# Kernel tuning notes

Hardware: AMD Instinct MI355X
Metric: run time of the kernel (lower is better)

## Reference

```python
import jax, jax.numpy as jnp
import numpy as np
from jax import lax

NH, K, V, TOPK = 8, 64, 64, 4  # n_heads, key_size, val_size, SparseAttention top_k(=3+1)
EPS = 1e-7
BN_EPS = 1e-5


def conv1x1(x, w, b):
    # x: [B,C,H,W], w: [O,C] -> [B,O,H,W]
    return jnp.einsum('oc,bchw->bohw', w, x) + b[None, :, None, None]


def conv3x3(x, w, b):
    y = lax.conv_general_dilated(x, w, (1, 1), 'SAME',
                                 dimension_numbers=('NCHW', 'OIHW', 'NCHW'))
    return y + b[None, :, None, None]


def batchnorm(x, g, b):
    # training-mode BN over (N,H,W), biased variance (matches torch BatchNorm2d in train)
    m = jnp.mean(x, axis=(0, 2, 3), keepdims=True)
    v = jnp.var(x, axis=(0, 2, 3), keepdims=True)
    return (x - m) * lax.rsqrt(v + BN_EPS) * g[None, :, None, None] + b[None, :, None, None]


def to_flat(y, d):
    # [B, NH*d, H, W] -> [B*H*W*NH, d]
    B, _, H, W = y.shape
    return y.reshape(B, NH, d, H, W).transpose(0, 3, 4, 1, 2).reshape(B * H * W * NH, d)


def setup_inputs() -> dict:
    key = jax.random.key(0)
    ks = jax.random.split(key, 16)
    L, C, B, H, W = 4, 256, 8, 32, 32
    KH, VH = K * NH, V * NH
    s = 0.02
    return {
        'x': jax.random.normal(ks[0], (B, C, H, W), jnp.float32),
        'kw': jax.random.normal(ks[1], (L, KH, C), jnp.float32) * s,
        'kb': jax.random.normal(ks[2], (L, KH), jnp.float32) * s,
        'qw': jax.random.normal(ks[3], (L, KH, C), jnp.float32) * s,
        'qb': jax.random.normal(ks[4], (L, KH), jnp.float32) * s,
        'vw': jax.random.normal(ks[5], (L, VH, C), jnp.float32) * s,
        'vb': jax.random.normal(ks[6], (L, VH), jnp.float32) * s,
        'ow1': jax.random.normal(ks[7], (L, C, VH, 3, 3), jnp.float32) * s,
        'ob1': jax.random.normal(ks[8], (L, C), jnp.float32) * s,
        'bn_g': jnp.ones((L, C), jnp.float32),
        'bn_b': jnp.zeros((L, C), jnp.float32),
        'ow2': jax.random.normal(ks[9], (L, C, C, 3, 3), jnp.float32) * s,
        'ob2': jax.random.normal(ks[10], (L, C), jnp.float32) * s,
        'gammas': jax.random.normal(ks[11], (L,), jnp.float32),
    }


def reference(x, kw, kb, qw, qb, vw, vb, ow1, ob1, bn_g, bn_b, ow2, ob2, gammas):
    B, C, H, W = x.shape
    L = kw.shape[0]
    temp = jnp.asarray(np.power(K, 0.5), x.dtype)  # concentration=0.5
    keys, vals = [], []
    for l in range(L):  # structurally distinct layers: growing key/val list
        keys.append(to_flat(conv1x1(x, kw[l], kb[l]), K))  # [N,K]
        vals.append(to_flat(conv1x1(x, vw[l], vb[l]), V))  # [N,V]
        q = to_flat(conv1x1(x, qw[l], qb[l]), K)           # [N,K]
        kt = jnp.stack(keys + [jnp.zeros_like(keys[0])], axis=1)  # [N,T,K] zero key appended
        vt = jnp.stack(vals + [jnp.zeros_like(vals[0])], axis=1)  # [N,T,V]
        scores = jnp.einsum('nk,ntk->nt', q / temp, kt)
        attn = jax.nn.softmax(scores, axis=-1)
        T = attn.shape[1]
        if T > TOPK:  # SparseAttention: topk threshold, clamp, renormalize
            delta = lax.top_k(attn, TOPK)[0][:, -1] + EPS
            wgt = jnp.maximum(attn - delta[:, None], 0.0)
            attn = wgt / (jnp.sum(wgt, axis=1, keepdims=True) + EPS)
        o = jnp.einsum('nt,ntv->nv', attn, vt)  # [N,V]
        o = o.reshape(B, H, W, NH * V).transpose(0, 3, 1, 2)  # [B, NH*V, H, W]
        h1 = jax.nn.relu(batchnorm(conv3x3(o, ow1[l], ob1[l]), bn_g[l], bn_b[l]))
        h2 = conv3x3(h1, ow2[l], ob2[l])
        x = x + h2 * gammas[l]
    return x
```

## Files before the change

### kernel.cpp

```cpp
#include <hip/hip_runtime.h>


typedef __attribute__((ext_vector_type(8))) short short8;
typedef __attribute__((ext_vector_type(4))) float f32x4;
typedef __attribute__((ext_vector_type(4))) unsigned short ushort4_t;
typedef __attribute__((ext_vector_type(4))) unsigned int uint4_t;

#define NTOK 65536
#define NPIX 8192

__device__ __forceinline__ float bf2f(unsigned short u) {
  unsigned int v = ((unsigned int)u) << 16;
  float f; __builtin_memcpy(&f, &v, 4); return f;
}
__device__ __forceinline__ unsigned short f2bf(float f) {
  unsigned int u; __builtin_memcpy(&u, &f, 4);
  u = (u + 0x7FFFu + ((u >> 16) & 1u)) >> 16;
  return (unsigned short)u;
}
__device__ __forceinline__ float blo(unsigned int u) {
  unsigned int v = u << 16; float f; __builtin_memcpy(&f, &v, 4); return f;
}
__device__ __forceinline__ float bhi(unsigned int u) {
  unsigned int v = u & 0xFFFF0000u; float f; __builtin_memcpy(&f, &v, 4); return f;
}

__device__ __forceinline__ void gl_lds16(const unsigned short* g, const unsigned short* l) {
  __builtin_amdgcn_global_load_lds(
      (const __attribute__((address_space(1))) unsigned int*)g,
      (__attribute__((address_space(3))) unsigned int*)l, 16, 0, 0);
}

__global__ void k_prep(const float* __restrict__ kw, const float* __restrict__ vw,
                       const float* __restrict__ qw, const float* __restrict__ ow1,
                       const float* __restrict__ ow2, const float* __restrict__ kb,
                       const float* __restrict__ vb, const float* __restrict__ qb,
                       unsigned short* __restrict__ wkqv, unsigned short* __restrict__ w1,
                       unsigned short* __restrict__ w2, float* __restrict__ biascat) {
  long i = (long)blockIdx.x * 256 + threadIdx.x;
  if (i < 1572864) {
    int idx = (int)(i & 131071); int sl = (int)(i >> 17); int slot = sl % 3, l = sl / 3;
    const float* s = slot == 0 ? kw : slot == 1 ? vw : qw;
    wkqv[i] = f2bf(s[(size_t)l * 131072 + idx]);
    return;
  }
  i -= 1572864;
  if (i < 4718592) {
    int c = (int)(i % 512), tap = (int)((i / 512) % 9); long m = i / 4608;
    w1[i] = f2bf(ow1[(m * 512 + c) * 9 + tap]);
    return;
  }
  i -= 4718592;
  if (i < 2359296) {
    int c = (int)(i % 256), tap = (int)((i / 256) % 9); long m = i / 2304;
    w2[i] = f2bf(ow2[(m * 256 + c) * 9 + tap]);
    return;
  }
  i -= 2359296;
  if (i < 6144) {
    int o = (int)(i & 511); int sl = (int)(i >> 9); int slot = sl % 3, l = sl / 3;
    const float* s = slot == 0 ? kb : slot == 1 ? vb : qb;
    biascat[i] = s[l * 512 + o];
  }
}

__global__ __launch_bounds__(256) void k_x2cl(const float* __restrict__ src,
                                              unsigned short* __restrict__ dst) {
  __shared__ unsigned short t[64][68];
  const int hw0 = blockIdx.x * 64, b = blockIdx.y;
  const int tid = threadIdx.x;
  for (int cc = 0; cc < 4; cc++) {
    __syncthreads();
    {
      const int px = tid & 63, c = tid >> 6;
      #pragma unroll
      for (int i = 0; i < 16; i++)
        t[px][c + i * 4] = f2bf(src[((size_t)b * 256 + cc * 64 + c + i * 4) * 1024 + hw0 + px]);
    }
    __syncthreads();
    {
      const int px = tid >> 2, c0 = (tid & 3) * 16;
      unsigned short* dp = dst + ((size_t)b * 1024 + hw0 + px) * 256 + cc * 64 + c0;
      short8 v0, v1;
      #pragma unroll
      for (int i = 0; i < 8; i++) { v0[i] = (short)t[px][c0 + i]; v1[i] = (short)t[px][c0 + 8 + i]; }
      *(short8*)dp = v0; *(short8*)(dp + 8) = v1;
    }
  }
}

template<int MODE, int NSTEP, int KDIM, int CIN>
__global__ __launch_bounds__(256) void k_gemm(
    const unsigned short* __restrict__ W,
    const unsigned short* __restrict__ act,
    const float* __restrict__ bias,
    int l,
    unsigned short* __restrict__ ktok, unsigned short* __restrict__ vtok,
    unsigned short* __restrict__ qtok,
    float* __restrict__ pout) {
  __shared__ unsigned short sm[2][2][8192];

  const int bid = blockIdx.x;
  int m0, b, pix0, s;
  if constexpr (MODE == 0) {
    const int xcd = bid & 7, li = bid >> 3;
    const int nt = xcd * 8 + (li & 7);
    m0 = (li >> 3) * 128; s = 0;
    b = nt >> 3; pix0 = (nt & 7) * 128;
  } else {
    const int xcd = bid & 7, li = bid >> 3;
    const int nt = xcd * 8 + (li & 7);
    const int r = li >> 3;
    m0 = (r & 1) * 128; s = r >> 1;
    b = nt >> 3; pix0 = (nt & 7) * 128;
  }
  constexpr int SW = (MODE == 1) ? 128 : 64;

  const int tid = threadIdx.x;
  const int wid = tid >> 6, lane = tid & 63;
  const int lr = lane & 15, lg = lane >> 4;
  const int m_off = (wid >> 1) * 64, n_off = (wid & 1) * 64;

  const unsigned short* gA[4];
  const unsigned short* gB[4];
  #pragma unroll
  for (int j = 0; j < 4; j++) {
    const int o = (wid * 4 + j) * 512 + lane * 8;
    const int row = o >> 6;
    const int ksw = (((o >> 3) & 7) ^ (row & 7)) * 8;
    gA[j] = W + (size_t)(m0 + row) * KDIM + (MODE ? s * SW : 0) + ksw;
    if constexpr (MODE == 0) {
      gB[j] = act + ((size_t)b * 1024 + pix0 + row) * 256 + ksw;
    } else {
      const int pix = pix0 + row, py = pix >> 5, px = pix & 31;
      gB[j] = act + (size_t)b * 1156 * CIN + ((size_t)py * 34 + px) * CIN + s * SW + ksw;
    }
  }

  auto offA = [&](int st) -> int {
    if constexpr (MODE == 0) return st * 64;
    else if constexpr (MODE == 1) return (st >> 1) * 512 + (st & 1) * 64;
    else return st * 256;
  };
  auto offB = [&](int st) -> int {
    if constexpr (MODE == 0) return st * 64;
    else if constexpr (MODE == 1) {
      const int tap = st >> 1, dy = tap / 3, dx = tap - dy * 3;
      return (dy * 34 + dx) * 512 + (st & 1) * 64;
    } else {
      const int dy = st / 3, dx = st - dy * 3;
      return (dy * 34 + dx) * 256;
    }
  };
  auto STAGE = [&](int bf, int st) {
    const int oa = offA(st), ob = offB(st);
    #pragma unroll
    for (int j = 0; j < 4; j++) gl_lds16(gA[j] + oa, &sm[bf][0][(wid * 4 + j) * 512]);
    #pragma unroll
    for (int j = 0; j < 4; j++) gl_lds16(gB[j] + ob, &sm[bf][1][(wid * 4 + j) * 512]);
  };

  f32x4 acc[4][4] = {};

  STAGE(0, 0);
  __syncthreads();
  #pragma unroll
  for (int st = 0; st < NSTEP; st++) {
    if (st + 1 < NSTEP) STAGE((st + 1) & 1, st + 1);
    const int cur = st & 1;
    #pragma unroll
    for (int ks = 0; ks < 2; ks++) {
      short8 af[4], bfr[4];
      #pragma unroll
      for (int i = 0; i < 4; i++) {
        const int ra = m_off + i * 16 + lr;
        af[i] = *(const short8*)&sm[cur][0][ra * 64 + (((ks * 4 + lg) ^ (ra & 7)) * 8)];
        const int rb = n_off + i * 16 + lr;
        bfr[i] = *(const short8*)&sm[cur][1][rb * 64 + (((ks * 4 + lg) ^ (rb & 7)) * 8)];
      }
      #pragma unroll
      for (int i = 0; i < 4; i++)
        #pragma unroll
        for (int jn = 0; jn < 4; jn++)
          acc[i][jn] = __builtin_amdgcn_mfma_f32_16x16x32_bf16(af[i], bfr[jn], acc[i][jn], 0, 0, 0);
    }
    __syncthreads();
  }

  if constexpr (MODE == 0) {
    #pragma unroll
    for (int mi = 0; mi < 4; mi++) {
      const int mb = m0 + m_off + mi * 16 + lg * 4;
      const int tensor = mb >> 9, head = (mb >> 6) & 7, d0 = mb & 63;
      unsigned short* dst = (tensor == 0) ? ktok + (size_t)l * NTOK * 64
                          : (tensor == 1) ? vtok + (size_t)l * NTOK * 64 : qtok;
      const float b0 = bias[mb], b1 = bias[mb + 1], b2 = bias[mb + 2], b3 = bias[mb + 3];
      #pragma unroll
      for (int ni = 0; ni < 4; ni++) {
        const int n = pix0 + n_off + ni * 16 + lr;
        ushort4_t pk;
        pk[0] = f2bf(acc[mi][ni][0] + b0); pk[1] = f2bf(acc[mi][ni][1] + b1);
        pk[2] = f2bf(acc[mi][ni][2] + b2); pk[3] = f2bf(acc[mi][ni][3] + b3);
        *(ushort4_t*)&dst[(((size_t)b * 1024 + n) * 8 + head) * 64 + d0] = pk;
      }
    }
  } else {
    #pragma unroll
    for (int mi = 0; mi < 4; mi++) {
      const int mb = m0 + m_off + mi * 16 + lg * 4;
      float* orow = pout + (size_t)(s * 256 + mb) * 8192 + (size_t)b * 1024 + pix0;
      #pragma unroll
      for (int ni = 0; ni < 4; ni++) {
        const int n = n_off + ni * 16 + lr;
        #pragma unroll
        for (int r = 0; r < 4; r++) orow[(size_t)r * 8192 + n] = acc[mi][ni][r];
      }
    }
  }
}

template<int L>
__global__ __launch_bounds__(256) void k_attn(const unsigned int* __restrict__ q_tok,
                                              const unsigned int* __restrict__ k_tok,
                                              const unsigned int* __restrict__ v_tok,
                                              unsigned int* __restrict__ opad) {
  constexpr int T = L + 2;
  const int lane = threadIdx.x & 63, wid = threadIdx.x >> 6;
  const int ti = lane >> 2, dq = lane & 3;
  const int token = blockIdx.x * 64 + wid * 16 + ti;
  const size_t rowq = (size_t)token * 32 + dq * 8;

  unsigned int q[8];
  *(uint4_t*)&q[0] = *(const uint4_t*)(q_tok + rowq);
  *(uint4_t*)&q[4] = *(const uint4_t*)(q_tok + rowq + 4);
  float qf[16];
  #pragma unroll
  for (int j = 0; j < 8; j++) {
    qf[2 * j]     = blo(q[j]) * 0.125f;
    qf[2 * j + 1] = bhi(q[j]) * 0.125f;
  }

  float s[T];
  s[T - 1] = 0.0f;
  #pragma unroll
  for (int t = 0; t <= L; t++) {
    const unsigned int* kp = k_tok + (size_t)t * (NTOK * 32) + rowq;
    unsigned int kk[8];
    *(uint4_t*)&kk[0] = *(const uint4_t*)kp;
    *(uint4_t*)&kk[4] = *(const uint4_t*)(kp + 4);
    float p = 0.0f;
    #pragma unroll
    for (int j = 0; j < 8; j++) {
      p = fmaf(qf[2 * j], blo(kk[j]), p);
      p = fmaf(qf[2 * j + 1], bhi(kk[j]), p);
    }
    p += __shfl_xor(p, 1);
    p += __shfl_xor(p, 2);
    s[t] = p;
  }

  float mx = s[0];
  #pragma unroll
  for (int t = 1; t < T; t++) mx = fmaxf(mx, s[t]);
  float attn[T], sum = 0.0f;
  #pragma unroll
  for (int t = 0; t < T; t++) { attn[t] = __expf(s[t] - mx); sum += attn[t]; }
  const float inv = 1.0f / sum;
  #pragma unroll
  for (int t = 0; t < T; t++) attn[t] *= inv;

  if constexpr (T == 5) {
    float m1 = attn[0], m2 = 1e30f;
    #pragma unroll
    for (int t = 1; t < 5; t++) {
      const float a = attn[t];
      const float nm1 = fminf(m1, a);
      m2 = fminf(m2, fmaxf(m1, a));
      m1 = nm1;
    }
    const float delta = m2 + 1e-7f;
    float ws = 0.0f;
    #pragma unroll
    for (int t = 0; t < 5; t++) { attn[t] = fmaxf(attn[t] - delta, 0.0f); ws += attn[t]; }
    const float r = 1.0f / (ws + 1e-7f);
    #pragma unroll
    for (int t = 0; t < 5; t++) attn[t] *= r;
  }

  float o[16];
  #pragma unroll
  for (int i = 0; i < 16; i++) o[i] = 0.0f;
  #pragma unroll
  for (int t = 0; t <= L; t++) {
    const unsigned int* vp = v_tok + (size_t)t * (NTOK * 32) + rowq;
    unsigned int vv[8];
    *(uint4_t*)&vv[0] = *(const uint4_t*)vp;
    *(uint4_t*)&vv[4] = *(const uint4_t*)(vp + 4);
    const float a = attn[t];
    #pragma unroll
    for (int j = 0; j < 8; j++) {
      o[2 * j]     = fmaf(a, blo(vv[j]), o[2 * j]);
      o[2 * j + 1] = fmaf(a, bhi(vv[j]), o[2 * j + 1]);
    }
  }

  unsigned int po[8];
  #pragma unroll
  for (int j = 0; j < 8; j++) {
    unsigned int r;
    asm("v_cvt_pk_bf16_f32 %0, %1, %2" : "=v"(r) : "v"(o[2 * j]), "v"(o[2 * j + 1]));
    po[j] = r;
  }
  const int head = token & 7, pix = token >> 3;
  const int b = pix >> 10, hw = pix & 1023, y = hw >> 5, x = hw & 31;
  unsigned int* dp = opad +
      (((size_t)b * 1156 + (y + 1) * 34 + (x + 1)) * 512 + head * 64 + dq * 16) / 2;
  *(uint4_t*)dp = *(uint4_t*)&po[0];
  *(uint4_t*)(dp + 4) = *(uint4_t*)&po[4];
}

__global__ __launch_bounds__(512) void k_comb_stats(const float* __restrict__ p,
    const float* __restrict__ bias1, const float* __restrict__ g, const float* __restrict__ bta,
    float* __restrict__ h1c, float* __restrict__ stats) {
  const int c = blockIdx.x, tid = threadIdx.x;
  const float bs = bias1[c];
  float s = 0.0f, ss = 0.0f;
  const float* p0 = p + (size_t)c * 8192;
  float* h0 = h1c + (size_t)c * 8192;
  for (int n = tid; n < 8192; n += 512) {
    float v = p0[n] + p0[n + 2097152] + p0[n + 4194304] + p0[n + 6291456] + bs;
    h0[n] = v; s += v; ss += v * v;
  }
  #pragma unroll
  for (int o = 32; o > 0; o >>= 1) { s += __shfl_xor(s, o); ss += __shfl_xor(ss, o); }
  __shared__ float rs[8], rss[8];
  const int wid = tid >> 6, lane = tid & 63;
  if (lane == 0) { rs[wid] = s; rss[wid] = ss; }
  __syncthreads();
  if (tid == 0) {
    float S = 0.0f, SS = 0.0f;
    #pragma unroll
    for (int w = 0; w < 8; w++) { S += rs[w]; SS += rss[w]; }
    const float m = S * (1.0f / 8192.0f);
    const float var = SS * (1.0f / 8192.0f) - m * m;
    const float A = g[c] * rsqrtf(var + 1e-5f);
    stats[c] = A;
    stats[256 + c] = bta[c] - m * A;
  }
}

__global__ __launch_bounds__(512) void k_bn_relu_pad(const float* __restrict__ h,
    const float* __restrict__ stats, unsigned short* __restrict__ hpad) {
  __shared__ unsigned short t[64][72];
  const int hw0 = blockIdx.x * 64, b = blockIdx.y, tid = threadIdx.x;
  for (int cc = 0; cc < 4; cc++) {
    __syncthreads();
    {
      const int px = tid & 63, c = tid >> 6;
      #pragma unroll
      for (int i = 0; i < 8; i++) {
        const int ch = cc * 64 + i * 8 + c;
        float v = h[(size_t)ch * 8192 + (size_t)b * 1024 + hw0 + px] * stats[ch] + stats[256 + ch];
        t[px][i * 8 + c] = f2bf(fmaxf(v, 0.0f));
      }
    }
    __syncthreads();
    {
      const int px = tid >> 3, c0 = (tid & 7) * 8;
      const int hw = hw0 + px, y = hw >> 5, x = hw & 31;
      short8 v;
      #pragma unroll
      for (int i = 0; i < 8; i++) v[i] = (short)t[px][c0 + i];
      *(short8*)&hpad[((size_t)b * 1156 + (y + 1) * 34 + (x + 1)) * 256 + cc * 64 + c0] = v;
    }
  }
}

__global__ __launch_bounds__(512) void k_comb2(const float* __restrict__ p,
    const float* __restrict__ bias2, const float* __restrict__ gamma_p, int last,
    float* __restrict__ xacc, unsigned short* __restrict__ xcl) {
  __shared__ unsigned short t[64][72];
  const int hw0 = blockIdx.x * 64, b = blockIdx.y, tid = threadIdx.x;
  const float g = gamma_p[0];
  for (int cc = 0; cc < 4; cc++) {
    __syncthreads();
    {
      const int px = tid & 63, c = tid >> 6;
      #pragma unroll
      for (int i = 0; i < 8; i++) {
        const int ch = cc * 64 + i * 8 + c;
        const size_t nb = (size_t)ch * 8192 + (size_t)b * 1024 + hw0 + px;
        float v = p[nb] + p[nb + 2097152] + p[nb + 4194304] + p[nb + 6291456] + bias2[ch];
        const size_t xi = ((size_t)b * 256 + ch) * 1024 + hw0 + px;
        const float xn = xacc[xi] + g * v;
        xacc[xi] = xn;
        t[px][i * 8 + c] = f2bf(xn);
      }
    }
    __syncthreads();
    if (!last) {
      const int px = tid >> 3, c0 = (tid & 7) * 8;
      short8 v;
      #pragma unroll
      for (int i = 0; i < 8; i++) v[i] = (short)t[px][c0 + i];
      *(short8*)&xcl[((size_t)b * 1024 + hw0 + px) * 256 + cc * 64 + c0] = v;
    }
  }
}

extern "C" void kernel_launch(void* const* d_in, const int* in_sizes, int n_in,
                              void* d_out, int out_size, void* d_ws, size_t ws_size,
                              hipStream_t stream) {
  (void)in_sizes; (void)n_in; (void)out_size;
  const float* x_in   = (const float*)d_in[0];
  const float* kw     = (const float*)d_in[1];
  const float* kb     = (const float*)d_in[2];
  const float* qw     = (const float*)d_in[3];
  const float* qb     = (const float*)d_in[4];
  const float* vw     = (const float*)d_in[5];
  const float* vb     = (const float*)d_in[6];
  const float* ow1    = (const float*)d_in[7];
  const float* ob1    = (const float*)d_in[8];
  const float* bn_g   = (const float*)d_in[9];
  const float* bn_b   = (const float*)d_in[10];
  const float* ow2    = (const float*)d_in[11];
  const float* ob2    = (const float*)d_in[12];
  const float* gammas = (const float*)d_in[13];

  char* ws = (char*)d_ws;
  size_t off = 0;
  auto alloc = [&](size_t bytes) -> void* {
    void* pp = ws + off;
    off += (bytes + 255) & ~(size_t)255;
    return pp;
  };
  unsigned short* xcl     = (unsigned short*)alloc((size_t)NPIX * 256 * 2);
  unsigned short* k_tok   = (unsigned short*)alloc((size_t)4 * NTOK * 64 * 2);
  unsigned short* v_tok   = (unsigned short*)alloc((size_t)4 * NTOK * 64 * 2);
  unsigned short* q_tok   = (unsigned short*)alloc((size_t)NTOK * 64 * 2);
  unsigned short* opad    = (unsigned short*)alloc((size_t)8 * 1156 * 512 * 2);
  float*          h1c     = (float*)alloc((size_t)256 * 8192 * 4);
  unsigned short* h1pad   = (unsigned short*)alloc((size_t)8 * 1156 * 256 * 2);
  float*          p1      = (float*)alloc((size_t)4 * 256 * 8192 * 4);
  float*          stats   = (float*)alloc(512 * 4);
  unsigned short* wkqv    = (unsigned short*)alloc((size_t)4 * 3 * 512 * 256 * 2);
  unsigned short* w1bf    = (unsigned short*)alloc((size_t)1024 * 4608 * 2);
  unsigned short* w2bf    = (unsigned short*)alloc((size_t)1024 * 2304 * 2);
  float*          biascat = (float*)alloc((size_t)6144 * 4);
  if (off > ws_size) return;

  float* xacc = (float*)d_out;

  hipMemsetAsync(opad, 0, (size_t)8 * 1156 * 512 * 2, stream);
  hipMemsetAsync(h1pad, 0, (size_t)8 * 1156 * 256 * 2, stream);
  hipMemcpyAsync(xacc, x_in, (size_t)NPIX * 256 * 4, hipMemcpyDeviceToDevice, stream);
  k_prep<<<33816, 256, 0, stream>>>(kw, vw, qw, ow1, ow2, kb, vb, qb,
                                    wkqv, w1bf, w2bf, biascat);
  k_x2cl<<<dim3(16, 8), 256, 0, stream>>>(x_in, xcl);

  for (int l = 0; l < 4; l++) {
    k_gemm<0, 4, 256, 256><<<768, 256, 0, stream>>>(
        wkqv + (size_t)l * 3 * 512 * 256, xcl, biascat + l * 1536, l,
        k_tok, v_tok, q_tok, nullptr);
    const unsigned int* qt = (const unsigned int*)q_tok;
    const unsigned int* kt = (const unsigned int*)k_tok;
    const unsigned int* vt = (const unsigned int*)v_tok;
    unsigned int* op = (unsigned int*)opad;
    switch (l) {
      case 0: k_attn<0><<<1024, 256, 0, stream>>>(qt, kt, vt, op); break;
      case 1: k_attn<1><<<1024, 256, 0, stream>>>(qt, kt, vt, op); break;
      case 2: k_attn<2><<<1024, 256, 0, stream>>>(qt, kt, vt, op); break;
      default: k_attn<3><<<1024, 256, 0, stream>>>(qt, kt, vt, op); break;
    }
    k_gemm<1, 18, 4608, 512><<<512, 256, 0, stream>>>(
        w1bf + (size_t)l * 256 * 4608, opad, nullptr, l,
        nullptr, nullptr, nullptr, p1);
    k_comb_stats<<<256, 512, 0, stream>>>(p1, ob1 + l * 256, bn_g + l * 256,
                                          bn_b + l * 256, h1c, stats);
    k_bn_relu_pad<<<dim3(16, 8), 512, 0, stream>>>(h1c, stats, h1pad);
    k_gemm<2, 9, 2304, 256><<<512, 256, 0, stream>>>(
        w2bf + (size_t)l * 256 * 2304, h1pad, nullptr, l,
        nullptr, nullptr, nullptr, p1);
    k_comb2<<<dim3(16, 8), 512, 0, stream>>>(p1, ob2 + l * 256, gammas + l,
                                             (l == 3) ? 1 : 0, xacc, xcl);
  }
}
```

Before: 390.7 us.

## Store conv split-K partials and BN intermediates in bf16, vectorize epilogues

```diff
diff --git a/kernel.cpp b/kernel.cpp
--- a/kernel.cpp
+++ b/kernel.cpp
@@ -89,6 +89,19 @@
   }
 }
 
+__global__ __launch_bounds__(256) void k_zero_borders(unsigned int* __restrict__ opad,
+                                                      unsigned int* __restrict__ h1pad) {
+  const int idx = blockIdx.x;
+  const int b = idx / 132, i = idx % 132;
+  int y, x;
+  if (i < 34) { y = 0; x = i; }
+  else if (i < 68) { y = 33; x = i - 34; }
+  else { const int j = i - 68; y = 1 + (j >> 1); x = (j & 1) * 33; }
+  const size_t pix = (size_t)b * 1156 + y * 34 + x;
+  opad[pix * 256 + threadIdx.x] = 0u;
+  if (threadIdx.x < 128) h1pad[pix * 128 + threadIdx.x] = 0u;
+}
+
 template<int MODE, int NSTEP, int KDIM, int CIN>
 __global__ __launch_bounds__(256) void k_gemm(
     const unsigned short* __restrict__ W,
@@ -97,7 +110,7 @@
     int l,
     unsigned short* __restrict__ ktok, unsigned short* __restrict__ vtok,
     unsigned short* __restrict__ qtok,
-    float* __restrict__ pout) {
+    unsigned short* __restrict__ pout) {
   __shared__ unsigned short sm[2][2][8192];
 
   const int bid = blockIdx.x;
@@ -208,12 +221,12 @@
     #pragma unroll
     for (int mi = 0; mi < 4; mi++) {
       const int mb = m0 + m_off + mi * 16 + lg * 4;
-      float* orow = pout + (size_t)(s * 256 + mb) * 8192 + (size_t)b * 1024 + pix0;
+      unsigned short* orow = pout + (size_t)(s * 256 + mb) * 8192 + (size_t)b * 1024 + pix0;
       #pragma unroll
       for (int ni = 0; ni < 4; ni++) {
         const int n = n_off + ni * 16 + lr;
         #pragma unroll
-        for (int r = 0; r < 4; r++) orow[(size_t)r * 8192 + n] = acc[mi][ni][r];
+        for (int r = 0; r < 4; r++) orow[(size_t)r * 8192 + n] = f2bf(acc[mi][ni][r]);
       }
     }
   }
@@ -319,28 +332,40 @@
   *(uint4_t*)(dp + 4) = *(uint4_t*)&po[4];
 }
 
-__global__ __launch_bounds__(512) void k_comb_stats(const float* __restrict__ p,
+__global__ __launch_bounds__(256) void k_comb_stats(const unsigned int* __restrict__ p,
     const float* __restrict__ bias1, const float* __restrict__ g, const float* __restrict__ bta,
-    float* __restrict__ h1c, float* __restrict__ stats) {
+    unsigned int* __restrict__ h1c, float* __restrict__ stats) {
   const int c = blockIdx.x, tid = threadIdx.x;
   const float bs = bias1[c];
+  const unsigned int* P0 = p + (size_t)c * 4096;
+  unsigned int* H = h1c + (size_t)c * 4096;
   float s = 0.0f, ss = 0.0f;
-  const float* p0 = p + (size_t)c * 8192;
-  float* h0 = h1c + (size_t)c * 8192;
-  for (int n = tid; n < 8192; n += 512) {
-    float v = p0[n] + p0[n + 2097152] + p0[n + 4194304] + p0[n + 6291456] + bs;
-    h0[n] = v; s += v; ss += v * v;
-  }
-  #pragma unroll
-  for (int o = 32; o > 0; o >>= 1) { s += __shfl_xor(s, o); ss += __shfl_xor(ss, o); }
-  __shared__ float rs[8], rss[8];
+  #pragma unroll
+  for (int k2 = 0; k2 < 4; k2++) {
+    const int j = (k2 * 256 + tid) * 4;
+    uint4_t a0 = *(const uint4_t*)(P0 + j);
+    uint4_t a1 = *(const uint4_t*)(P0 + 1048576 + j);
+    uint4_t a2 = *(const uint4_t*)(P0 + 2097152 + j);
+    uint4_t a3 = *(const uint4_t*)(P0 + 3145728 + j);
+    uint4_t o;
+    #pragma unroll
+    for (int e = 0; e < 4; e++) {
+      const float vl = blo(a0[e]) + blo(a1[e]) + blo(a2[e]) + blo(a3[e]) + bs;
+      const float vh = bhi(a0[e]) + bhi(a1[e]) + bhi(a2[e]) + bhi(a3[e]) + bs;
+      s += vl + vh; ss += vl * vl + vh * vh;
+      o[e] = (unsigned int)f2bf(vl) | ((unsigned int)f2bf(vh) << 16);
+    }
+    *(uint4_t*)(H + j) = o;
+  }
+  #pragma unroll
+  for (int o2 = 32; o2 > 0; o2 >>= 1) { s += __shfl_xor(s, o2); ss += __shfl_xor(ss, o2); }
+  __shared__ float rs[4], rss[4];
   const int wid = tid >> 6, lane = tid & 63;
   if (lane == 0) { rs[wid] = s; rss[wid] = ss; }
   __syncthreads();
   if (tid == 0) {
-    float S = 0.0f, SS = 0.0f;
-    #pragma unroll
-    for (int w = 0; w < 8; w++) { S += rs[w]; SS += rss[w]; }
+    const float S = rs[0] + rs[1] + rs[2] + rs[3];
+    const float SS = rss[0] + rss[1] + rss[2] + rss[3];
     const float m = S * (1.0f / 8192.0f);
     const float var = SS * (1.0f / 8192.0f) - m * m;
     const float A = g[c] * rsqrtf(var + 1e-5f);
@@ -349,61 +374,80 @@
   }
 }
 
-__global__ __launch_bounds__(512) void k_bn_relu_pad(const float* __restrict__ h,
+__global__ __launch_bounds__(256) void k_bn_relu_pad(const unsigned int* __restrict__ h1c,
     const float* __restrict__ stats, unsigned short* __restrict__ hpad) {
-  __shared__ unsigned short t[64][72];
-  const int hw0 = blockIdx.x * 64, b = blockIdx.y, tid = threadIdx.x;
-  for (int cc = 0; cc < 4; cc++) {
-    __syncthreads();
-    {
-      const int px = tid & 63, c = tid >> 6;
-      #pragma unroll
-      for (int i = 0; i < 8; i++) {
-        const int ch = cc * 64 + i * 8 + c;
-        float v = h[(size_t)ch * 8192 + (size_t)b * 1024 + hw0 + px] * stats[ch] + stats[256 + ch];
-        t[px][i * 8 + c] = f2bf(fmaxf(v, 0.0f));
-      }
-    }
-    __syncthreads();
-    {
-      const int px = tid >> 3, c0 = (tid & 7) * 8;
-      const int hw = hw0 + px, y = hw >> 5, x = hw & 31;
-      short8 v;
-      #pragma unroll
-      for (int i = 0; i < 8; i++) v[i] = (short)t[px][c0 + i];
-      *(short8*)&hpad[((size_t)b * 1156 + (y + 1) * 34 + (x + 1)) * 256 + cc * 64 + c0] = v;
-    }
-  }
-}
-
-__global__ __launch_bounds__(512) void k_comb2(const float* __restrict__ p,
+  __shared__ unsigned short t[32][264];
+  const int hw0 = blockIdx.x * 32, b = blockIdx.y, tid = threadIdx.x;
+  const int c = tid;
+  const float A = stats[c], Bt = stats[256 + c];
+  const unsigned int* src = h1c + (size_t)c * 4096 + ((size_t)b * 1024 + hw0) / 2;
+  #pragma unroll
+  for (int k2 = 0; k2 < 4; k2++) {
+    uint4_t a = *(const uint4_t*)(src + k2 * 4);
+    #pragma unroll
+    for (int e = 0; e < 4; e++) {
+      const int px = k2 * 8 + e * 2;
+      t[px][c]     = f2bf(fmaxf(blo(a[e]) * A + Bt, 0.0f));
+      t[px + 1][c] = f2bf(fmaxf(bhi(a[e]) * A + Bt, 0.0f));
+    }
+  }
+  __syncthreads();
+  const int px = tid >> 3, c0 = (tid & 7) * 32;
+  const int y = hw0 >> 5, x = (hw0 & 31) + px;
+  unsigned short* dp = hpad + ((size_t)b * 1156 + (y + 1) * 34 + (x + 1)) * 256 + c0;
+  #pragma unroll
+  for (int q = 0; q < 4; q++) {
+    short8 v;
+    #pragma unroll
+    for (int i = 0; i < 8; i++) v[i] = (short)t[px][c0 + q * 8 + i];
+    *(short8*)(dp + q * 8) = v;
+  }
+}
+
+__global__ __launch_bounds__(256) void k_comb2(const unsigned int* __restrict__ p,
     const float* __restrict__ bias2, const float* __restrict__ gamma_p, int last,
     float* __restrict__ xacc, unsigned short* __restrict__ xcl) {
-  __shared__ unsigned short t[64][72];
-  const int hw0 = blockIdx.x * 64, b = blockIdx.y, tid = threadIdx.x;
-  const float g = gamma_p[0];
-  for (int cc = 0; cc < 4; cc++) {
-    __syncthreads();
-    {
-      const int px = tid & 63, c = tid >> 6;
-      #pragma unroll
-      for (int i = 0; i < 8; i++) {
-        const int ch = cc * 64 + i * 8 + c;
-        const size_t nb = (size_t)ch * 8192 + (size_t)b * 1024 + hw0 + px;
-        float v = p[nb] + p[nb + 2097152] + p[nb + 4194304] + p[nb + 6291456] + bias2[ch];
-        const size_t xi = ((size_t)b * 256 + ch) * 1024 + hw0 + px;
-        const float xn = xacc[xi] + g * v;
-        xacc[xi] = xn;
-        t[px][i * 8 + c] = f2bf(xn);
-      }
-    }
-    __syncthreads();
-    if (!last) {
-      const int px = tid >> 3, c0 = (tid & 7) * 8;
+  __shared__ unsigned short t[32][264];
+  const int hw0 = blockIdx.x * 32, b = blockIdx.y, tid = threadIdx.x;
+  const int c = tid;
+  const float gmm = gamma_p[0], bs = bias2[c];
+  const unsigned int* P0 = p + (size_t)c * 4096 + ((size_t)b * 1024 + hw0) / 2;
+  float* X = xacc + ((size_t)b * 256 + c) * 1024 + hw0;
+  #pragma unroll
+  for (int k2 = 0; k2 < 4; k2++) {
+    uint4_t a0 = *(const uint4_t*)(P0 + k2 * 4);
+    uint4_t a1 = *(const uint4_t*)(P0 + 1048576 + k2 * 4);
+    uint4_t a2 = *(const uint4_t*)(P0 + 2097152 + k2 * 4);
+    uint4_t a3 = *(const uint4_t*)(P0 + 3145728 + k2 * 4);
+    f32x4 x0 = *(const f32x4*)(X + k2 * 8);
+    f32x4 x1 = *(const f32x4*)(X + k2 * 8 + 4);
+    float xn[8];
+    #pragma unroll
+    for (int e = 0; e < 4; e++) {
+      const float vl = blo(a0[e]) + blo(a1[e]) + blo(a2[e]) + blo(a3[e]) + bs;
+      const float vh = bhi(a0[e]) + bhi(a1[e]) + bhi(a2[e]) + bhi(a3[e]) + bs;
+      const float xl = (e < 2 ? x0[2 * e] : x1[2 * e - 4]);
+      const float xh = (e < 2 ? x0[2 * e + 1] : x1[2 * e - 3]);
+      xn[2 * e]     = xl + gmm * vl;
+      xn[2 * e + 1] = xh + gmm * vh;
+    }
+    f32x4 w0 = {xn[0], xn[1], xn[2], xn[3]};
+    f32x4 w1 = {xn[4], xn[5], xn[6], xn[7]};
+    *(f32x4*)(X + k2 * 8) = w0;
+    *(f32x4*)(X + k2 * 8 + 4) = w1;
+    #pragma unroll
+    for (int i = 0; i < 8; i++) t[k2 * 8 + i][c] = f2bf(xn[i]);
+  }
+  __syncthreads();
+  if (!last) {
+    const int px = tid >> 3, c0 = (tid & 7) * 32;
+    unsigned short* dp = xcl + ((size_t)b * 1024 + hw0 + px) * 256 + c0;
+    #pragma unroll
+    for (int q = 0; q < 4; q++) {
       short8 v;
       #pragma unroll
-      for (int i = 0; i < 8; i++) v[i] = (short)t[px][c0 + i];
-      *(short8*)&xcl[((size_t)b * 1024 + hw0 + px) * 256 + cc * 64 + c0] = v;
+      for (int i = 0; i < 8; i++) v[i] = (short)t[px][c0 + q * 8 + i];
+      *(short8*)(dp + q * 8) = v;
     }
   }
 }
@@ -439,9 +483,9 @@
   unsigned short* v_tok   = (unsigned short*)alloc((size_t)4 * NTOK * 64 * 2);
   unsigned short* q_tok   = (unsigned short*)alloc((size_t)NTOK * 64 * 2);
   unsigned short* opad    = (unsigned short*)alloc((size_t)8 * 1156 * 512 * 2);
-  float*          h1c     = (float*)alloc((size_t)256 * 8192 * 4);
+  unsigned int*   h1c     = (unsigned int*)alloc((size_t)256 * 4096 * 4);
   unsigned short* h1pad   = (unsigned short*)alloc((size_t)8 * 1156 * 256 * 2);
-  float*          p1      = (float*)alloc((size_t)4 * 256 * 8192 * 4);
+  unsigned short* p1      = (unsigned short*)alloc((size_t)4 * 256 * 8192 * 2);
   float*          stats   = (float*)alloc(512 * 4);
   unsigned short* wkqv    = (unsigned short*)alloc((size_t)4 * 3 * 512 * 256 * 2);
   unsigned short* w1bf    = (unsigned short*)alloc((size_t)1024 * 4608 * 2);
@@ -451,8 +495,7 @@
 
   float* xacc = (float*)d_out;
 
-  hipMemsetAsync(opad, 0, (size_t)8 * 1156 * 512 * 2, stream);
-  hipMemsetAsync(h1pad, 0, (size_t)8 * 1156 * 256 * 2, stream);
+  k_zero_borders<<<1056, 256, 0, stream>>>((unsigned int*)opad, (unsigned int*)h1pad);
   hipMemcpyAsync(xacc, x_in, (size_t)NPIX * 256 * 4, hipMemcpyDeviceToDevice, stream);
   k_prep<<<33816, 256, 0, stream>>>(kw, vw, qw, ow1, ow2, kb, vb, qb,
                                     wkqv, w1bf, w2bf, biascat);
@@ -475,13 +518,13 @@
     k_gemm<1, 18, 4608, 512><<<512, 256, 0, stream>>>(
         w1bf + (size_t)l * 256 * 4608, opad, nullptr, l,
         nullptr, nullptr, nullptr, p1);
-    k_comb_stats<<<256, 512, 0, stream>>>(p1, ob1 + l * 256, bn_g + l * 256,
-                                          bn_b + l * 256, h1c, stats);
-    k_bn_relu_pad<<<dim3(16, 8), 512, 0, stream>>>(h1c, stats, h1pad);
+    k_comb_stats<<<256, 256, 0, stream>>>((const unsigned int*)p1, ob1 + l * 256,
+                                          bn_g + l * 256, bn_b + l * 256, h1c, stats);
+    k_bn_relu_pad<<<dim3(32, 8), 256, 0, stream>>>(h1c, stats, h1pad);
     k_gemm<2, 9, 2304, 256><<<512, 256, 0, stream>>>(
         w2bf + (size_t)l * 256 * 2304, h1pad, nullptr, l,
         nullptr, nullptr, nullptr, p1);
-    k_comb2<<<dim3(16, 8), 512, 0, stream>>>(p1, ob2 + l * 256, gammas + l,
-                                             (l == 3) ? 1 : 0, xacc, xcl);
-  }
-}
+    k_comb2<<<dim3(32, 8), 256, 0, stream>>>((const unsigned int*)p1, ob2 + l * 256,
+                                             gammas + l, (l == 3) ? 1 : 0, xacc, xcl);
+  }
+}
```

Result: slower. 414.4 us (+6.1%).
